# Performance work log

Measured on AMD Instinct MI355X. Metric: run time of the kernel, lower is better.

The kernel has to match this reference:

```python
import jax, jax.numpy as jnp
import numpy as np


def setup_inputs() -> dict:
    key = jax.random.key(0)
    k1, k2 = jax.random.split(key)
    # input: (B, T, C, H, W)
    x = jax.random.normal(k1, (8, 16, 64, 64, 64), dtype=jnp.float32)
    # ConvLSTM gate conv weight: (4*hidden_dim, input_dim + hidden_dim, 3, 3), bias=False
    Wk = jax.random.normal(k2, (256, 128, 3, 3), dtype=jnp.float32) * 0.05
    return {"x": x, "Wk": Wk}


def reference(x, Wk):
    b, t, c, h, w = x.shape
    hd = Wk.shape[0] // 4  # hidden_dim

    def step(carry, xt):
        hid, cell = carry
        z = jnp.concatenate([xt, hid], axis=1)  # (B, C+HD, H, W)
        conv = jax.lax.conv_general_dilated(
            z, Wk, window_strides=(1, 1), padding='SAME',
            dimension_numbers=('NCHW', 'OIHW', 'NCHW'))  # (B, 4*HD, H, W)
        cc_i, cc_f, cc_o, cc_g = jnp.split(conv, 4, axis=1)
        i = jax.nn.sigmoid(cc_i)
        f = jax.nn.sigmoid(cc_f)
        o = jax.nn.sigmoid(cc_o)
        g = jnp.tanh(cc_g)
        cell = f * cell + i * g
        hid = o * jnp.tanh(cell)
        return (hid, cell), None

    h0 = jnp.zeros((b, hd, h, w), dtype=x.dtype)
    c0 = jnp.zeros_like(h0)
    (hid, cell), _ = jax.lax.scan(step, (h0, c0), jnp.swapaxes(x, 0, 1))
    return hid, cell
```

## Files before the change

kernel.cpp:

```cpp
#include <hip/hip_runtime.h>
#include <cmath>


#define CHW 262144
#define ZSZ 12960

typedef short bf16x8 __attribute__((ext_vector_type(8)));
typedef float f32x4  __attribute__((ext_vector_type(4)));

static __device__ __forceinline__ ushort f2bf(float f) {
    union { float f; unsigned u; } v; v.f = f;
    unsigned u = v.u;
    return (ushort)((u + 0x7FFFu + ((u >> 16) & 1u)) >> 16);
}
static __device__ __forceinline__ float bf2f(ushort u) {
    union { unsigned u; float f; } v; v.u = (unsigned)u << 16; return v.f;
}
static __device__ __forceinline__ float sigf(float x) {
    return 1.f / (1.f + __expf(-x));
}

__global__ void transform_w(const float* __restrict__ Wk, ushort* __restrict__ Wt) {
    const int idx  = blockIdx.x * 256 + threadIdx.x;
    const int lane = idx & 63;
    const int g    = (idx >> 6) & 3;
    const int r2   = idx >> 8;
    const int tap  = r2 % 9;
    const int cq   = r2 / 9;
    const int q    = cq & 3;
    const int cix  = cq >> 2;
    const int oc   = g * 64 + q * 16 + (lane & 15);
    const int icb  = cix * 32 + (lane >> 4) * 8;
    const int ky   = tap / 3, kx = tap - ky * 3;
    ushort* dst = Wt + (size_t)idx * 8;
    #pragma unroll
    for (int j = 0; j < 8; ++j)
        dst[j] = f2bf(Wk[((size_t)(oc * 128 + icb + j) * 3 + ky) * 3 + kx]);
}

__global__ __launch_bounds__(256) void xconv(const float* __restrict__ x,
                                             ushort* __restrict__ xb) {
    __shared__ ushort T[256 * 66];
    const int tid = threadIdx.x;
    const int pg  = blockIdx.x;
    const int bt  = blockIdx.y;
    const float* xt = x  + (size_t)bt * CHW;
    ushort*      xo = xb + (size_t)bt * CHW;
    const int p0 = pg * 256;
    #pragma unroll
    for (int ch = 0; ch < 64; ++ch)
        T[tid * 66 + ch] = f2bf(xt[(size_t)ch * 4096 + p0 + tid]);
    __syncthreads();
    #pragma unroll
    for (int k = 0; k < 64; ++k) {
        const int item = k * 256 + tid;
        const int px = item >> 6, ch = item & 63;
        xo[(size_t)(p0 + px) * 64 + ch] = T[px * 66 + ch];
    }
}

static __device__ __forceinline__ void stage_chunk(
    ushort* __restrict__ dst, const ushort* __restrict__ src,
    int tid, int ty0, int tx0) {
    #pragma unroll
    for (int k = 0; k < 11; ++k) {
        const int i = tid + k * 256;
        if (i < 2592) {
            const int p   = i >> 3;
            const int icq = i & 7;
            const int py  = p / 18;
            const int pxl = p - py * 18;
            const int gy  = ty0 + py - 1;
            const int gx  = tx0 + pxl - 1;
            ushort4 v = {0, 0, 0, 0};
            if (((unsigned)gy < 64u) & ((unsigned)gx < 64u))
                v = *(const ushort4*)&src[(size_t)(gy * 64 + gx) * 64 + icq * 4];
            *(ushort4*)&dst[p * 40 + icq * 4] = v;
        }
    }
}

__global__ __launch_bounds__(256) void convlstm_step(
    const ushort* __restrict__ xb,
    const ushort* __restrict__ Wt,
    const ushort* __restrict__ hin,
    ushort*       __restrict__ hout,
    float*        __restrict__ cell,
    int t, int first)
{
    __shared__ __align__(16) ushort zs[2 * ZSZ];

    const int tid  = threadIdx.x;
    const int lane = tid & 63;
    const int w    = tid >> 6;
    const int col  = lane & 15;
    const int quad = lane >> 4;
    const int q8   = quad * 8;

    const int tile = blockIdx.x;
    const int ty0  = (tile >> 2) * 16;
    const int tx0  = (tile & 3) * 16;
    const int q    = blockIdx.y;
    const int hc0  = q * 16;
    const int b    = blockIdx.z;

    const ushort* xt = xb + ((size_t)b * 16 + t) * CHW;
    const ushort* hb = hin + (size_t)b * CHW;
    float*        cb = cell + (size_t)b * CHW;
    ushort*       ho = hout + (size_t)b * CHW;

    const int gy_ = ty0 + 4 * w;
    const int gx_ = tx0 + quad * 4;

    const ushort* wq = Wt + (size_t)q * 18432;

    f32x4 cpv[4];
    #pragma unroll
    for (int r = 0; r < 4; ++r)
        #pragma unroll
        for (int reg = 0; reg < 4; ++reg)
            cpv[r][reg] = first ? 0.f
                : cb[((size_t)(gy_ + r) * 64 + gx_ + reg) * 64 + hc0 + col];

    f32x4 acc[4][4];
    #pragma unroll
    for (int r = 0; r < 4; ++r)
        #pragma unroll
        for (int g = 0; g < 4; ++g)
            acc[r][g] = (f32x4){0.f, 0.f, 0.f, 0.f};

    stage_chunk(zs, xt, tid, ty0, tx0);
    __syncthreads();

    #pragma unroll
    for (int cix = 0; cix < 4; ++cix) {
        ushort* cur = zs + (cix & 1) * ZSZ;
        ushort* nxt = zs + ((cix + 1) & 1) * ZSZ;

        if (cix == 0) stage_chunk(nxt, xt + 32, tid, ty0, tx0);
        else if (cix == 1) stage_chunk(nxt, hb, tid, ty0, tx0);
        else if (cix == 2) stage_chunk(nxt, hb + 32, tid, ty0, tx0);

        const ushort* wb = wq + (size_t)cix * 4 * 18432;
        #pragma unroll
        for (int kx = 0; kx < 3; ++kx) {
            bf16x8 arow[6];
            #pragma unroll
            for (int j = 0; j < 6; ++j)
                arow[j] = *(const bf16x8*)&cur[((4 * w + j) * 18 + col + kx) * 40 + q8];
            #pragma unroll
            for (int ky = 0; ky < 3; ++ky) {
                const int tap = ky * 3 + kx;
                bf16x8 bfr[4];
                #pragma unroll
                for (int g = 0; g < 4; ++g)
                    bfr[g] = *(const bf16x8*)(wb + (size_t)tap * 2048 + g * 512 + lane * 8);
                #pragma unroll
                for (int g = 0; g < 4; ++g)
                    #pragma unroll
                    for (int r = 0; r < 4; ++r)
                        acc[r][g] = __builtin_amdgcn_mfma_f32_16x16x32_bf16(
                            arow[r + ky], bfr[g], acc[r][g], 0, 0, 0);
            }
        }
        __syncthreads();
    }

    #pragma unroll
    for (int r = 0; r < 4; ++r) {
        const size_t rowbase = ((size_t)(gy_ + r) * 64 + gx_) * 64 + hc0 + col;
        #pragma unroll
        for (int reg = 0; reg < 4; ++reg) {
            const float ci = acc[r][0][reg];
            const float cf = acc[r][1][reg];
            const float co = acc[r][2][reg];
            const float cg = acc[r][3][reg];
            const float cn = sigf(cf) * cpv[r][reg] + sigf(ci) * tanhf(cg);
            const float hn = sigf(co) * tanhf(cn);
            cb[rowbase + (size_t)reg * 64] = cn;
            ho[rowbase + (size_t)reg * 64] = f2bf(hn);
        }
    }
}

__global__ __launch_bounds__(256) void conv_out(
    const ushort* __restrict__ hN, const float* __restrict__ cN,
    float* __restrict__ out)
{
    __shared__ float T[64][65];
    const int tid  = threadIdx.x;
    const int pg   = blockIdx.x;
    const int b    = blockIdx.y;
    const int tsel = blockIdx.z;
    const int pix0 = pg * 64;

    #pragma unroll
    for (int k = 0; k < 16; ++k) {
        const int idx = k * 256 + tid;
        const int pl = idx >> 6, ch = idx & 63;
        const size_t src = (size_t)b * CHW + (size_t)(pix0 + pl) * 64 + ch;
        T[pl][ch] = tsel ? cN[src] : bf2f(hN[src]);
    }
    __syncthreads();
    float* base = out + (tsel ? 2097152 : 0);
    #pragma unroll
    for (int k = 0; k < 16; ++k) {
        const int idx = k * 256 + tid;
        const int ch = idx >> 6, pl = idx & 63;
        base[(size_t)b * CHW + (size_t)ch * 4096 + pix0 + pl] = T[pl][ch];
    }
}

extern "C" void kernel_launch(void* const* d_in, const int* in_sizes, int n_in,
                              void* d_out, int out_size, void* d_ws, size_t ws_size,
                              hipStream_t stream) {
    const float* x  = (const float*)d_in[0];
    const float* Wk = (const float*)d_in[1];
    float* out = (float*)d_out;

    char* ws = (char*)d_ws;
    ushort* Wt   = (ushort*)ws;
    float*  cb   = (float*)(ws + (1u << 20));
    ushort* hb0  = (ushort*)(ws + (16u << 20));
    ushort* hb1  = (ushort*)(ws + (20u << 20));
    ushort* xb   = (ushort*)(ws + (32u << 20));

    (void)hipMemsetAsync(hb0, 0, 4194304, stream);
    transform_w<<<144, 256, 0, stream>>>(Wk, Wt);
    xconv<<<dim3(16, 128), 256, 0, stream>>>(x, xb);

    dim3 grid(16, 4, 8);
    for (int t = 0; t < 16; ++t) {
        const ushort* hi = (t & 1) ? hb1 : hb0;
        ushort*       ho = (t & 1) ? hb0 : hb1;
        convlstm_step<<<grid, 256, 0, stream>>>(xb, Wt, hi, ho, cb, t, t == 0);
    }
    conv_out<<<dim3(64, 8, 2), 256, 0, stream>>>(hb0, cb, out);
}
```

Before: 712.0 us.

## Fuse all timesteps into one persistent kernel with a grid barrier

Replaces the 16 per-timestep launches with a single persistent kernel that loops over time and synchronises all 512 blocks through an atomic-counter grid barrier in workspace memory. The cell state now stays in registers across steps and is written to global memory only at the final step, which removes per-step cell reads and writes as well as launch gaps. The design depends on all 512 blocks being co-resident (launch bounds set to 2 blocks per SM). If they are not, the spin barrier deadlocks, and the barrier itself adds per-step latency.

```diff
diff --git a/kernel.cpp b/kernel.cpp
--- a/kernel.cpp
+++ b/kernel.cpp
@@ -4,6 +4,7 @@
 
 #define CHW 262144
 #define ZSZ 12960
+#define NBLK 512u
 
 typedef short bf16x8 __attribute__((ext_vector_type(8)));
 typedef float f32x4  __attribute__((ext_vector_type(4)));
@@ -80,13 +81,13 @@
     }
 }
 
-__global__ __launch_bounds__(256) void convlstm_step(
+__global__ __launch_bounds__(256, 2) void convlstm_all(
     const ushort* __restrict__ xb,
     const ushort* __restrict__ Wt,
-    const ushort* __restrict__ hin,
-    ushort*       __restrict__ hout,
+    ushort*       __restrict__ hb0,
+    ushort*       __restrict__ hb1,
     float*        __restrict__ cell,
-    int t, int first)
+    unsigned*     __restrict__ bar)
 {
     __shared__ __align__(16) ushort zs[2 * ZSZ];
 
@@ -104,81 +105,96 @@
     const int hc0  = q * 16;
     const int b    = blockIdx.z;
 
-    const ushort* xt = xb + ((size_t)b * 16 + t) * CHW;
-    const ushort* hb = hin + (size_t)b * CHW;
-    float*        cb = cell + (size_t)b * CHW;
-    ushort*       ho = hout + (size_t)b * CHW;
+    ushort* h0 = hb0 + (size_t)b * CHW;
+    ushort* h1 = hb1 + (size_t)b * CHW;
+    float*  cb = cell + (size_t)b * CHW;
 
     const int gy_ = ty0 + 4 * w;
     const int gx_ = tx0 + quad * 4;
-
     const ushort* wq = Wt + (size_t)q * 18432;
 
     f32x4 cpv[4];
     #pragma unroll
     for (int r = 0; r < 4; ++r)
+        cpv[r] = (f32x4){0.f, 0.f, 0.f, 0.f};
+
+    for (int t = 0; t < 16; ++t) {
+        const ushort* xt = xb + ((size_t)b * 16 + t) * CHW;
+        const ushort* hi = (t & 1) ? h1 : h0;
+        ushort*       ho = (t & 1) ? h0 : h1;
+
+        f32x4 acc[4][4];
         #pragma unroll
-        for (int reg = 0; reg < 4; ++reg)
-            cpv[r][reg] = first ? 0.f
-                : cb[((size_t)(gy_ + r) * 64 + gx_ + reg) * 64 + hc0 + col];
-
-    f32x4 acc[4][4];
-    #pragma unroll
-    for (int r = 0; r < 4; ++r)
+        for (int r = 0; r < 4; ++r)
+            #pragma unroll
+            for (int g = 0; g < 4; ++g)
+                acc[r][g] = (f32x4){0.f, 0.f, 0.f, 0.f};
+
+        stage_chunk(zs, xt, tid, ty0, tx0);
+        __syncthreads();
+
         #pragma unroll
-        for (int g = 0; g < 4; ++g)
-            acc[r][g] = (f32x4){0.f, 0.f, 0.f, 0.f};
-
-    stage_chunk(zs, xt, tid, ty0, tx0);
-    __syncthreads();
-
-    #pragma unroll
-    for (int cix = 0; cix < 4; ++cix) {
-        ushort* cur = zs + (cix & 1) * ZSZ;
-        ushort* nxt = zs + ((cix + 1) & 1) * ZSZ;
-
-        if (cix == 0) stage_chunk(nxt, xt + 32, tid, ty0, tx0);
-        else if (cix == 1) stage_chunk(nxt, hb, tid, ty0, tx0);
-        else if (cix == 2) stage_chunk(nxt, hb + 32, tid, ty0, tx0);
-
-        const ushort* wb = wq + (size_t)cix * 4 * 18432;
+        for (int cix = 0; cix < 4; ++cix) {
+            ushort* cur = zs + (cix & 1) * ZSZ;
+            ushort* nxt = zs + ((cix + 1) & 1) * ZSZ;
+
+            if (cix == 0) stage_chunk(nxt, xt + 32, tid, ty0, tx0);
+            else if (cix == 1) stage_chunk(nxt, hi, tid, ty0, tx0);
+            else if (cix == 2) stage_chunk(nxt, hi + 32, tid, ty0, tx0);
+
+            const ushort* wb = wq + (size_t)cix * 4 * 18432;
+            #pragma unroll
+            for (int kx = 0; kx < 3; ++kx) {
+                bf16x8 arow[6];
+                #pragma unroll
+                for (int j = 0; j < 6; ++j)
+                    arow[j] = *(const bf16x8*)&cur[((4 * w + j) * 18 + col + kx) * 40 + q8];
+                #pragma unroll
+                for (int ky = 0; ky < 3; ++ky) {
+                    const int tap = ky * 3 + kx;
+                    bf16x8 bfr[4];
+                    #pragma unroll
+                    for (int g = 0; g < 4; ++g)
+                        bfr[g] = *(const bf16x8*)(wb + (size_t)tap * 2048 + g * 512 + lane * 8);
+                    #pragma unroll
+                    for (int g = 0; g < 4; ++g)
+                        #pragma unroll
+                        for (int r = 0; r < 4; ++r)
+                            acc[r][g] = __builtin_amdgcn_mfma_f32_16x16x32_bf16(
+                                arow[r + ky], bfr[g], acc[r][g], 0, 0, 0);
+                }
+            }
+            __syncthreads();
+        }
+
         #pragma unroll
-        for (int kx = 0; kx < 3; ++kx) {
-            bf16x8 arow[6];
+        for (int r = 0; r < 4; ++r) {
+            const size_t rowbase = ((size_t)(gy_ + r) * 64 + gx_) * 64 + hc0 + col;
             #pragma unroll
-            for (int j = 0; j < 6; ++j)
-                arow[j] = *(const bf16x8*)&cur[((4 * w + j) * 18 + col + kx) * 40 + q8];
-            #pragma unroll
-            for (int ky = 0; ky < 3; ++ky) {
-                const int tap = ky * 3 + kx;
-                bf16x8 bfr[4];
-                #pragma unroll
-                for (int g = 0; g < 4; ++g)
-                    bfr[g] = *(const bf16x8*)(wb + (size_t)tap * 2048 + g * 512 + lane * 8);
-                #pragma unroll
-                for (int g = 0; g < 4; ++g)
-                    #pragma unroll
-                    for (int r = 0; r < 4; ++r)
-                        acc[r][g] = __builtin_amdgcn_mfma_f32_16x16x32_bf16(
-                            arow[r + ky], bfr[g], acc[r][g], 0, 0, 0);
+            for (int reg = 0; reg < 4; ++reg) {
+                const float ci  = acc[r][0][reg];
+                const float cf  = acc[r][1][reg];
+                const float co  = acc[r][2][reg];
+                const float cgv = acc[r][3][reg];
+                const float cn  = sigf(cf) * cpv[r][reg] + sigf(ci) * tanhf(cgv);
+                const float hn  = sigf(co) * tanhf(cn);
+                cpv[r][reg] = cn;
+                ho[rowbase + (size_t)reg * 64] = f2bf(hn);
+                if (t == 15) cb[rowbase + (size_t)reg * 64] = cn;
             }
         }
-        __syncthreads();
-    }
-
-    #pragma unroll
-    for (int r = 0; r < 4; ++r) {
-        const size_t rowbase = ((size_t)(gy_ + r) * 64 + gx_) * 64 + hc0 + col;
-        #pragma unroll
-        for (int reg = 0; reg < 4; ++reg) {
-            const float ci = acc[r][0][reg];
-            const float cf = acc[r][1][reg];
-            const float co = acc[r][2][reg];
-            const float cg = acc[r][3][reg];
-            const float cn = sigf(cf) * cpv[r][reg] + sigf(ci) * tanhf(cg);
-            const float hn = sigf(co) * tanhf(cn);
-            cb[rowbase + (size_t)reg * 64] = cn;
-            ho[rowbase + (size_t)reg * 64] = f2bf(hn);
+
+        if (t < 15) {
+            __syncthreads();
+            if (tid == 0) {
+                __threadfence();
+                atomicAdd(&bar[t], 1u);
+                while (__hip_atomic_load(&bar[t], __ATOMIC_RELAXED,
+                                         __HIP_MEMORY_SCOPE_AGENT) < NBLK)
+                    __builtin_amdgcn_s_sleep(2);
+            }
+            __syncthreads();
+            __threadfence();
         }
     }
 }
@@ -219,21 +235,19 @@
     float* out = (float*)d_out;
 
     char* ws = (char*)d_ws;
-    ushort* Wt   = (ushort*)ws;
-    float*  cb   = (float*)(ws + (1u << 20));
-    ushort* hb0  = (ushort*)(ws + (16u << 20));
-    ushort* hb1  = (ushort*)(ws + (20u << 20));
-    ushort* xb   = (ushort*)(ws + (32u << 20));
+    ushort*   Wt  = (ushort*)ws;
+    unsigned* bar = (unsigned*)(ws + 917504);
+    float*    cb  = (float*)(ws + (1u << 20));
+    ushort*   hb0 = (ushort*)(ws + (16u << 20));
+    ushort*   hb1 = (ushort*)(ws + (20u << 20));
+    ushort*   xb  = (ushort*)(ws + (32u << 20));
 
     (void)hipMemsetAsync(hb0, 0, 4194304, stream);
+    (void)hipMemsetAsync(bar, 0, 64, stream);
     transform_w<<<144, 256, 0, stream>>>(Wk, Wt);
     xconv<<<dim3(16, 128), 256, 0, stream>>>(x, xb);
 
-    dim3 grid(16, 4, 8);
-    for (int t = 0; t < 16; ++t) {
-        const ushort* hi = (t & 1) ? hb1 : hb0;
-        ushort*       ho = (t & 1) ? hb0 : hb1;
-        convlstm_step<<<grid, 256, 0, stream>>>(xb, Wt, hi, ho, cb, t, t == 0);
-    }
+    convlstm_all<<<dim3(16, 4, 8), 256, 0, stream>>>(xb, Wt, hb0, hb1, cb, bar);
+
     conv_out<<<dim3(64, 8, 2), 256, 0, stream>>>(hb0, cb, out);
 }
```

New measurement: 2.662 ms. 274% more time.
